# Optimization experiments

Measured on AMD Instinct MI355X. Metric: run time of the kernel, lower is better.

## Reference

```python
import jax, jax.numpy as jnp
import numpy as np

# SqueezeSeg CRF config
NUM_CLASS = 4
SIZE_Z, SIZE_A = 3, 5            # LCN_HEIGHT, LCN_WIDTH
B, H, W = 16, 64, 512            # batch, zenith, azimuth
RCRF_ITER = 3
BI_FILTER_COEF = 0.1
ANG_FILTER_COEF = 0.02
ANG_THETA_A = 0.9
BILATERAL_THETA_A = 0.9
K = SIZE_Z * SIZE_A              # 15 -> 14 neighbors (center excluded)

# neighbor offsets of the 3x5 condensing kernel, center excluded
OFFSETS = [(dz, da) for dz in range(SIZE_Z) for da in range(SIZE_A)
           if not (dz == SIZE_Z // 2 and da == SIZE_A // 2)]

def _gauss_weights(theta_sq):
    # angular_filter_kernel: Gaussian of squared spatial offset, center zeroed
    g = [np.exp(-((dz - SIZE_Z // 2) ** 2 + (da - SIZE_A // 2) ** 2) / (2.0 * theta_sq))
         for dz, da in OFFSETS]
    return jnp.asarray(np.array(g, dtype=np.float32))

def gather_neighbors(x):
    # x: [B,C,H,W] -> [B,C,K-1,H,W]; zero-padded 'same' neighborhood gather
    pz, pa = SIZE_Z // 2, SIZE_A // 2
    xp = jnp.pad(x, ((0, 0), (0, 0), (pz, pz), (pa, pa)))
    return jnp.stack([xp[:, :, dz:dz + H, da:da + W] for dz, da in OFFSETS], axis=2)

def setup_inputs() -> dict:
    key = jax.random.key(0)
    k1, k2, k3 = jax.random.split(key, 3)
    x = jax.random.normal(k1, (B, NUM_CLASS, H, W), dtype=jnp.float32)
    bilateral_filters = jax.random.uniform(k2, (B, 1, K - 1, H, W), dtype=jnp.float32)
    lidar_mask = (jax.random.uniform(k3, (B, 1, H, W)) > 0.5).astype(jnp.float32)
    return {"x": x, "bilateral_filters": bilateral_filters, "lidar_mask": lidar_mask}

def reference(x, bilateral_filters, lidar_mask):
    g_ang = _gauss_weights(ANG_THETA_A ** 2)
    g_bi = _gauss_weights(BILATERAL_THETA_A ** 2)
    compat = jnp.ones((NUM_CLASS, NUM_CLASS), jnp.float32) - jnp.eye(NUM_CLASS, dtype=jnp.float32)
    ang_compat = compat * ANG_FILTER_COEF   # [out_class, in_class] 1x1 conv
    bi_compat = compat * BI_FILTER_COEF

    for _ in range(RCRF_ITER):
        unary = jax.nn.softmax(x, axis=1)                     # softmax over class dim
        nb = gather_neighbors(unary)                          # [B,C,14,H,W]
        # depthwise angular filters = Gaussian-weighted neighbor sums
        ang = jnp.einsum('k,bckhw->bchw', g_ang, nb)
        bi_ang = jnp.einsum('k,bckhw->bchw', g_bi, nb)
        # condensing conv on masked unary, weighted by per-pixel bilateral filters
        nb_m = gather_neighbors(unary * lidar_mask)           # [B,C,14,H,W]
        condensed = jnp.sum(nb_m * bilateral_filters, axis=2) # [B,C,H,W]
        bi = condensed * lidar_mask * bi_ang
        # 1x1 compatibility transforms
        ang2 = jnp.einsum('oc,bchw->bohw', ang_compat, ang)
        bi2 = jnp.einsum('oc,bchw->bohw', bi_compat, bi)
        x = unary + ang2 + bi2
    return x
```

## Files before the change

### kernel.cpp

```cpp
#include <hip/hip_runtime.h>


#define NCLASS 4
#define HH 64
#define WW 512
#define BB 16
#define TH 8
#define TW 64
#define UR (TH + 6)
#define UC (TW + 12)
#define PLANE (HH * WW)
#define R1H 12
#define R1W 72
#define GPR1 (R1W / 2)
#define NPAIR1 (R1H * GPR1)

#define G1 0.53940412f
#define G2 0.29095687f
#define G4 0.08466190f
#define G5 0.04566227f

__device__ __forceinline__ void fma4(float4& d, float s, const float4& v) {
    d.x = fmaf(s, v.x, d.x);
    d.y = fmaf(s, v.y, d.y);
    d.z = fmaf(s, v.z, d.z);
    d.w = fmaf(s, v.w, d.w);
}

template <bool SM>
__device__ __forceinline__ float4 crf_combine(const float4 A, const float4 C,
                                              const float4 u, const float mcen)
{
    const float bx = C.x * mcen * A.x;
    const float by = C.y * mcen * A.y;
    const float bz = C.z * mcen * A.z;
    const float bw = C.w * mcen * A.w;
    const float sa = A.x + A.y + A.z + A.w;
    const float sb = bx + by + bz + bw;
    float4 r;
    r.x = u.x + 0.02f * (sa - A.x) + 0.1f * (sb - bx);
    r.y = u.y + 0.02f * (sa - A.y) + 0.1f * (sb - by);
    r.z = u.z + 0.02f * (sa - A.z) + 0.1f * (sb - bz);
    r.w = u.w + 0.02f * (sa - A.w) + 0.1f * (sb - bw);
    if (SM) {
        const float mx  = fmaxf(fmaxf(r.x, r.y), fmaxf(r.z, r.w));
        const float e0  = __expf(r.x - mx);
        const float e1  = __expf(r.y - mx);
        const float e2  = __expf(r.z - mx);
        const float e3  = __expf(r.w - mx);
        const float inv = 1.0f / (e0 + e1 + e2 + e3);
        r = make_float4(e0 * inv, e1 * inv, e2 * inv, e3 * inv);
    }
    return r;
}

template <int MR, int MC, bool FINAL>
__device__ __forceinline__ void crf_step(
    float4 (*__restrict__ u_lds)[UC], const float (*__restrict__ m_lds)[UC],
    const float2* __restrict__ f, float* __restrict__ dst,
    int b, int lr1, int lc1, int gh, int gw, bool inb)
{
    constexpr int RH = TH + 2 * MR;
    constexpr int RW = TW + 2 * MC;
    constexpr int LR_LO = 2 - MR, LR_HI = 2 - MR + RH;
    constexpr int LC_LO = 4 - MC, LC_HI = 4 - MC + RW;

    const bool act = inb && lr1 >= LR_LO && lr1 < LR_HI
                         && lc1 >= LC_LO && (lc1 + 1) < LC_HI;

    const float GE[5] = {G5, G2, G1, G2, G5};
    const float GC[5] = {G4, G1, 0.f, G1, G4};

    float4 r0 = make_float4(0.f, 0.f, 0.f, 0.f);
    float4 r1 = r0;

    if (act) {
        const int ur = lr1 + 1;
        const int uc = lc1 + 2;

        float4 A0 = make_float4(0.f, 0.f, 0.f, 0.f);
        float4 A1 = A0, C0 = A0, C1 = A0;
        float4 ucen0 = A0, ucen1 = A0;
        float  mcen0 = 0.f, mcen1 = 0.f;

#pragma unroll
        for (int dz = -1; dz <= 1; ++dz) {
            const int rr = ur + dz;
            float4 U[6];
            float  M[6];
#pragma unroll
            for (int t = 0; t < 6; ++t) U[t] = u_lds[rr][uc - 2 + t];
#pragma unroll
            for (int t = 0; t < 3; ++t) {
                const float2 mm =
                    *reinterpret_cast<const float2*>(&m_lds[rr][uc - 2 + 2 * t]);
                M[2 * t]     = mm.x;
                M[2 * t + 1] = mm.y;
            }
            if (dz == 0) { ucen0 = U[2]; ucen1 = U[3]; mcen0 = M[2]; mcen1 = M[3]; }
#pragma unroll
            for (int t = 0; t < 5; ++t) {
                if (dz == 0 && t == 2) continue;
                const int   k  = (dz == -1) ? t
                               : (dz == 0)  ? 5 + (t > 2 ? t - 1 : t)
                                            : 9 + t;
                const float gk = (dz == 0) ? GC[t] : GE[t];
                const float fm0 = f[k].x * M[t];
                const float fm1 = f[k].y * M[t + 1];
                fma4(A0, gk,  U[t]);      fma4(C0, fm0, U[t]);
                fma4(A1, gk,  U[t + 1]);  fma4(C1, fm1, U[t + 1]);
            }
        }
        r0 = crf_combine<!FINAL>(A0, C0, ucen0, mcen0);
        r1 = crf_combine<!FINAL>(A1, C1, ucen1, mcen1);

        if (FINAL) {
            float* o = dst + ((size_t)b * NCLASS * HH + gh) * WW + gw;
            *reinterpret_cast<float2*>(o)             = make_float2(r0.x, r1.x);
            *reinterpret_cast<float2*>(o + PLANE)     = make_float2(r0.y, r1.y);
            *reinterpret_cast<float2*>(o + 2 * PLANE) = make_float2(r0.z, r1.z);
            *reinterpret_cast<float2*>(o + 3 * PLANE) = make_float2(r0.w, r1.w);
        }
    }

    if (!FINAL) {
        __syncthreads();
        if (act) {
            u_lds[lr1 + 1][lc1 + 2] = r0;
            u_lds[lr1 + 1][lc1 + 3] = r1;
        }
        __syncthreads();
    }
}

__global__ __launch_bounds__(512, 4) void crf_fused(
    const float* __restrict__ xin,
    const float* __restrict__ filt,
    const float* __restrict__ mask,
    float* __restrict__ xout)
{
    __shared__ float4 u_lds[UR][UC];
    __shared__ float  m_lds[UR][UC];

    const int b   = blockIdx.z;
    const int h0  = blockIdx.y * TH;
    const int w0  = blockIdx.x * TW;
    const int tid = threadIdx.x;

    constexpr int NP = (UR * UC) / 2;
    for (int idx = tid; idx < NP; idx += 512) {
        const int lr = idx / (UC / 2);
        const int lc = 2 * (idx - lr * (UC / 2));
        const int ph = h0 + lr - 3;
        const int pw = w0 + lc - 6;
        float4 u0 = make_float4(0.f, 0.f, 0.f, 0.f);
        float4 u1 = u0;
        float2 mm = make_float2(0.f, 0.f);
        if (ph >= 0 && ph < HH && pw >= 0 && pw < WW) {
            const float* px = xin + ((size_t)b * NCLASS * HH + ph) * WW + pw;
            const float2 v0 = *reinterpret_cast<const float2*>(px);
            const float2 v1 = *reinterpret_cast<const float2*>(px + PLANE);
            const float2 v2 = *reinterpret_cast<const float2*>(px + 2 * PLANE);
            const float2 v3 = *reinterpret_cast<const float2*>(px + 3 * PLANE);
            mm = *reinterpret_cast<const float2*>(mask + ((size_t)b * HH + ph) * WW + pw);
            {
                const float mx  = fmaxf(fmaxf(v0.x, v1.x), fmaxf(v2.x, v3.x));
                const float e0  = __expf(v0.x - mx);
                const float e1  = __expf(v1.x - mx);
                const float e2  = __expf(v2.x - mx);
                const float e3  = __expf(v3.x - mx);
                const float inv = 1.0f / (e0 + e1 + e2 + e3);
                u0 = make_float4(e0 * inv, e1 * inv, e2 * inv, e3 * inv);
            }
            {
                const float mx  = fmaxf(fmaxf(v0.y, v1.y), fmaxf(v2.y, v3.y));
                const float e0  = __expf(v0.y - mx);
                const float e1  = __expf(v1.y - mx);
                const float e2  = __expf(v2.y - mx);
                const float e3  = __expf(v3.y - mx);
                const float inv = 1.0f / (e0 + e1 + e2 + e3);
                u1 = make_float4(e0 * inv, e1 * inv, e2 * inv, e3 * inv);
            }
        }
        u_lds[lr][lc]     = u0;
        u_lds[lr][lc + 1] = u1;
        *reinterpret_cast<float2*>(&m_lds[lr][lc]) = mm;
    }
    __syncthreads();

    const int  p   = tid;
    const int  lr1 = p / GPR1;
    const int  lc1 = 2 * (p - lr1 * GPR1);
    const int  gh  = h0 + lr1 - 2;
    const int  gw  = w0 + lc1 - 4;
    const bool inb = (p < NPAIR1) && gh >= 0 && gh < HH && gw >= 0 && gw < WW;

    float2 f[14];
    if (inb) {
        const float* fp = filt + ((size_t)b * 14 * HH + gh) * WW + gw;
#pragma unroll
        for (int k = 0; k < 14; ++k)
            f[k] = *reinterpret_cast<const float2*>(fp + (size_t)k * PLANE);
    }

    crf_step<2, 4, false>(u_lds, m_lds, f, xout, b, lr1, lc1, gh, gw, inb);
    crf_step<1, 2, false>(u_lds, m_lds, f, xout, b, lr1, lc1, gh, gw, inb);
    crf_step<0, 0, true >(u_lds, m_lds, f, xout, b, lr1, lc1, gh, gw, inb);
}

extern "C" void kernel_launch(void* const* d_in, const int* in_sizes, int n_in,
                              void* d_out, int out_size, void* d_ws, size_t ws_size,
                              hipStream_t stream) {
    const float* x    = (const float*)d_in[0];
    const float* filt = (const float*)d_in[1];
    const float* msk  = (const float*)d_in[2];
    float* out = (float*)d_out;
    (void)d_ws; (void)ws_size;

    dim3 grid(WW / TW, HH / TH, BB);
    dim3 block(512);
    crf_fused<<<grid, block, 0, stream>>>(x, filt, msk, out);
}
```

Measured before the change: 96.14 us.

## Premultiply mask into filters, separate Gaussian stencil, hoist filter loads before softmax

Folds the lidar mask values into the per-pixel bilateral filter weights once, so the three CRF iterations no longer reload mask values from LDS or multiply by them. The angular Gaussian sum becomes a vertical column sum followed by horizontal weights, with the centre term subtracted afterwards, which cuts FMAs per pixel pair. The global loads of the filter weights move ahead of the LDS fill loop so their latency overlaps the softmax work. The ang and bi_ang sums still share one accumulator because both Gaussians use the same theta. Adding the centre and then subtracting it changes rounding slightly.

```diff
diff --git a/kernel.cpp b/kernel.cpp
--- a/kernel.cpp
+++ b/kernel.cpp
@@ -56,8 +56,9 @@
 
 template <int MR, int MC, bool FINAL>
 __device__ __forceinline__ void crf_step(
-    float4 (*__restrict__ u_lds)[UC], const float (*__restrict__ m_lds)[UC],
-    const float2* __restrict__ f, float* __restrict__ dst,
+    float4 (*__restrict__ u_lds)[UC],
+    const float2* __restrict__ fm, float mcen0, float mcen1,
+    float* __restrict__ dst,
     int b, int lr1, int lc1, int gh, int gw, bool inb)
 {
     constexpr int RH = TH + 2 * MR;
@@ -68,8 +69,7 @@
     const bool act = inb && lr1 >= LR_LO && lr1 < LR_HI
                          && lc1 >= LC_LO && (lc1 + 1) < LC_HI;
 
-    const float GE[5] = {G5, G2, G1, G2, G5};
-    const float GC[5] = {G4, G1, 0.f, G1, G4};
+    const float GA[5] = {G4, G1, 1.0f, G1, G4};
 
     float4 r0 = make_float4(0.f, 0.f, 0.f, 0.f);
     float4 r1 = r0;
@@ -81,36 +81,42 @@
         float4 A0 = make_float4(0.f, 0.f, 0.f, 0.f);
         float4 A1 = A0, C0 = A0, C1 = A0;
         float4 ucen0 = A0, ucen1 = A0;
-        float  mcen0 = 0.f, mcen1 = 0.f;
-
-#pragma unroll
-        for (int dz = -1; dz <= 1; ++dz) {
-            const int rr = ur + dz;
-            float4 U[6];
-            float  M[6];
-#pragma unroll
-            for (int t = 0; t < 6; ++t) U[t] = u_lds[rr][uc - 2 + t];
-#pragma unroll
-            for (int t = 0; t < 3; ++t) {
-                const float2 mm =
-                    *reinterpret_cast<const float2*>(&m_lds[rr][uc - 2 + 2 * t]);
-                M[2 * t]     = mm.x;
-                M[2 * t + 1] = mm.y;
-            }
-            if (dz == 0) { ucen0 = U[2]; ucen1 = U[3]; mcen0 = M[2]; mcen1 = M[3]; }
-#pragma unroll
-            for (int t = 0; t < 5; ++t) {
-                if (dz == 0 && t == 2) continue;
-                const int   k  = (dz == -1) ? t
-                               : (dz == 0)  ? 5 + (t > 2 ? t - 1 : t)
-                                            : 9 + t;
-                const float gk = (dz == 0) ? GC[t] : GE[t];
-                const float fm0 = f[k].x * M[t];
-                const float fm1 = f[k].y * M[t + 1];
-                fma4(A0, gk,  U[t]);      fma4(C0, fm0, U[t]);
-                fma4(A1, gk,  U[t + 1]);  fma4(C1, fm1, U[t + 1]);
-            }
-        }
+
+#pragma unroll
+        for (int t = 0; t < 6; ++t) {
+            const float4 Um = u_lds[ur - 1][uc - 2 + t];
+            const float4 Uc = u_lds[ur    ][uc - 2 + t];
+            const float4 Up = u_lds[ur + 1][uc - 2 + t];
+            float4 cv;
+            cv.x = fmaf(G1, Um.x + Up.x, Uc.x);
+            cv.y = fmaf(G1, Um.y + Up.y, Uc.y);
+            cv.z = fmaf(G1, Um.z + Up.z, Uc.z);
+            cv.w = fmaf(G1, Um.w + Up.w, Uc.w);
+            if (t == 2) ucen0 = Uc;
+            if (t == 3) ucen1 = Uc;
+            if (t < 5)  fma4(A0, GA[t],     cv);
+            if (t >= 1) fma4(A1, GA[t - 1], cv);
+            if (t < 5) {
+                fma4(C0, fm[t].x,     Um);
+                fma4(C0, fm[9 + t].x, Up);
+                if (t != 2) {
+                    const int kc = 5 + (t > 2 ? t - 1 : t);
+                    fma4(C0, fm[kc].x, Uc);
+                }
+            }
+            if (t >= 1) {
+                const int t1 = t - 1;
+                fma4(C1, fm[t1].y,     Um);
+                fma4(C1, fm[9 + t1].y, Up);
+                if (t1 != 2) {
+                    const int kc = 5 + (t1 > 2 ? t1 - 1 : t1);
+                    fma4(C1, fm[kc].y, Uc);
+                }
+            }
+        }
+        A0.x -= ucen0.x; A0.y -= ucen0.y; A0.z -= ucen0.z; A0.w -= ucen0.w;
+        A1.x -= ucen1.x; A1.y -= ucen1.y; A1.z -= ucen1.z; A1.w -= ucen1.w;
+
         r0 = crf_combine<!FINAL>(A0, C0, ucen0, mcen0);
         r1 = crf_combine<!FINAL>(A1, C1, ucen1, mcen1);
 
@@ -146,6 +152,21 @@
     const int h0  = blockIdx.y * TH;
     const int w0  = blockIdx.x * TW;
     const int tid = threadIdx.x;
+
+    const int  p   = tid;
+    const int  lr1 = p / GPR1;
+    const int  lc1 = 2 * (p - lr1 * GPR1);
+    const int  gh  = h0 + lr1 - 2;
+    const int  gw  = w0 + lc1 - 4;
+    const bool inb = (p < NPAIR1) && gh >= 0 && gh < HH && gw >= 0 && gw < WW;
+
+    float2 f[14];
+    if (inb) {
+        const float* fp = filt + ((size_t)b * 14 * HH + gh) * WW + gw;
+#pragma unroll
+        for (int k = 0; k < 14; ++k)
+            f[k] = *reinterpret_cast<const float2*>(fp + (size_t)k * PLANE);
+    }
 
     constexpr int NP = (UR * UC) / 2;
     for (int idx = tid; idx < NP; idx += 512) {
@@ -188,24 +209,38 @@
     }
     __syncthreads();
 
-    const int  p   = tid;
-    const int  lr1 = p / GPR1;
-    const int  lc1 = 2 * (p - lr1 * GPR1);
-    const int  gh  = h0 + lr1 - 2;
-    const int  gw  = w0 + lc1 - 4;
-    const bool inb = (p < NPAIR1) && gh >= 0 && gh < HH && gw >= 0 && gw < WW;
-
-    float2 f[14];
+    float mcen0 = 0.f, mcen1 = 0.f;
     if (inb) {
-        const float* fp = filt + ((size_t)b * 14 * HH + gh) * WW + gw;
-#pragma unroll
-        for (int k = 0; k < 14; ++k)
-            f[k] = *reinterpret_cast<const float2*>(fp + (size_t)k * PLANE);
-    }
-
-    crf_step<2, 4, false>(u_lds, m_lds, f, xout, b, lr1, lc1, gh, gw, inb);
-    crf_step<1, 2, false>(u_lds, m_lds, f, xout, b, lr1, lc1, gh, gw, inb);
-    crf_step<0, 0, true >(u_lds, m_lds, f, xout, b, lr1, lc1, gh, gw, inb);
+        const int ur = lr1 + 1;
+        const int uc = lc1 + 2;
+        mcen0 = m_lds[ur][uc];
+        mcen1 = m_lds[ur][uc + 1];
+#pragma unroll
+        for (int dz = -1; dz <= 1; ++dz) {
+            const int rr = ur + dz;
+            float M[6];
+#pragma unroll
+            for (int t3 = 0; t3 < 3; ++t3) {
+                const float2 mm =
+                    *reinterpret_cast<const float2*>(&m_lds[rr][uc - 2 + 2 * t3]);
+                M[2 * t3]     = mm.x;
+                M[2 * t3 + 1] = mm.y;
+            }
+#pragma unroll
+            for (int t = 0; t < 5; ++t) {
+                if (dz == 0 && t == 2) continue;
+                const int k = (dz == -1) ? t
+                            : (dz == 0)  ? 5 + (t > 2 ? t - 1 : t)
+                                         : 9 + t;
+                f[k].x *= M[t];
+                f[k].y *= M[t + 1];
+            }
+        }
+    }
+
+    crf_step<2, 4, false>(u_lds, f, mcen0, mcen1, xout, b, lr1, lc1, gh, gw, inb);
+    crf_step<1, 2, false>(u_lds, f, mcen0, mcen1, xout, b, lr1, lc1, gh, gw, inb);
+    crf_step<0, 0, true >(u_lds, f, mcen0, mcen1, xout, b, lr1, lc1, gh, gw, inb);
 }
 
 extern "C" void kernel_launch(void* const* d_in, const int* in_sizes, int n_in,
```

New measurement: 106.3 us. 10.5% more time.
